# Performance work log

Measured on AMD Instinct MI355X. Metric: run time of the kernel, lower is better.

Reference implementation:

```python
import jax, jax.numpy as jnp
import numpy as np

SEQ, PREV, BS, D_IN, H, D = 512, 512, 8, 1024, 16, 64


def setup_inputs() -> dict:
    key = jax.random.key(0)
    ks = jax.random.split(key, 10)
    s = 0.02
    inp = {
        "input_": jax.random.normal(ks[0], (SEQ, BS, D_IN), jnp.float32),
        "pos_embs": jax.random.normal(ks[1], (SEQ + PREV, D_IN), jnp.float32),
        "memory": jax.random.normal(ks[2], (PREV, BS, D_IN), jnp.float32),
        "u": jax.random.normal(ks[3], (H, D), jnp.float32) * s,
        "v": jax.random.normal(ks[4], (H, D), jnp.float32) * s,
        # causal mask allowing full attention to memory: triu with diagonal=1+prev
        "mask": (jnp.triu(jnp.ones((SEQ, SEQ + PREV), jnp.bool_), k=1 + PREV))[..., None],
        "W_kv": jax.random.normal(ks[5], (D_IN, 2 * H * D), jnp.float32) * s,
        "W_q": jax.random.normal(ks[6], (D_IN, H * D), jnp.float32) * s,
        "W_p": jax.random.normal(ks[7], (D_IN, H * D), jnp.float32) * s,
        "W_out": jax.random.normal(ks[8], (H * D, D_IN), jnp.float32) * s,
        "ln_gamma": jnp.ones((D_IN,), jnp.float32),
        "ln_beta": jnp.zeros((D_IN,), jnp.float32),
    }
    return inp


def _rel_shift(x):
    # x: (q, k, bs, H) -> pad one zero column, reshape-transpose trick, drop first row
    q, k, bs, h = x.shape
    zp = jnp.zeros((q, 1, bs, h), x.dtype)
    return jnp.concatenate([zp, x], axis=1).reshape(k + 1, q, bs, h)[1:].reshape(q, k, bs, h)


def reference(input_, pos_embs, memory, u, v, mask, W_kv, W_q, W_p, W_out, ln_gamma, ln_beta):
    cur_seq, bs, d_in = input_.shape
    prev_seq = memory.shape[0]
    tot = cur_seq + prev_seq
    h, d = u.shape
    scale = 1.0 / d ** 0.5

    iwm = jnp.concatenate([memory, input_], axis=0)          # (tot, bs, d_in)
    kv = jnp.einsum('jbe,ef->jbf', iwm, W_kv)                 # (tot, bs, 2*H*d)
    k_t, v_t = jnp.split(kv, 2, axis=-1)
    q_t = jnp.einsum('ibe,ef->ibf', input_, W_q)              # (cur, bs, H*d)

    q4 = q_t.reshape(cur_seq, bs, h, d)
    k4 = k_t.reshape(tot, bs, h, d)
    v4 = v_t.reshape(tot, bs, h, d)

    content_attn = jnp.einsum('ibhd,jbhd->ijbh', q4 + u, k4)  # (cur, tot, bs, H)

    p_t = (pos_embs @ W_p).reshape(tot, h, d)                 # (tot, H, d)
    position_attn = jnp.einsum('ibhd,jhd->ijbh', q4 + v, p_t)
    position_attn = _rel_shift(position_attn)

    attn = content_attn + position_attn
    attn = jnp.where(mask[..., None], -jnp.inf, attn)         # mask: (cur, tot, 1) -> (cur, tot, 1, 1)
    attn = jax.nn.softmax(attn * scale, axis=1)

    awv = jnp.einsum('ijbh,jbhd->ibhd', attn, v4).reshape(cur_seq, bs, h * d)
    out = input_ + awv @ W_out                                # residual

    mu = jnp.mean(out, axis=-1, keepdims=True)
    var = jnp.mean((out - mu) ** 2, axis=-1, keepdims=True)
    out = (out - mu) / jnp.sqrt(var + 1e-5) * ln_gamma + ln_beta
    return out
```

## Files before the change

kernel.cpp:

```cpp
#include <hip/hip_runtime.h>
#include <math.h>

#define SEQ  512
#define PREV 512
#define TOT  1024
#define BSZ  8
#define DIN  1024
#define NH   16
#define HD   64

typedef __bf16 bf16;
typedef __bf16 bf16x8 __attribute__((ext_vector_type(8)));
typedef float  f32x4  __attribute__((ext_vector_type(4)));
typedef float  f32x16 __attribute__((ext_vector_type(16)));
typedef unsigned int u32;
typedef u32 u32x2 __attribute__((ext_vector_type(2)));

__device__ __forceinline__ f32x4 MFMA16(bf16x8 a, bf16x8 b, f32x4 c) {
    return __builtin_amdgcn_mfma_f32_16x16x32_bf16(a, b, c, 0, 0, 0);
}
__device__ __forceinline__ f32x16 MFMA32(bf16x8 a, bf16x8 b, f32x16 c) {
    return __builtin_amdgcn_mfma_f32_32x32x16_bf16(a, b, c, 0, 0, 0);
}

#define GLOAD16(g, l) __builtin_amdgcn_global_load_lds( \
    (const __attribute__((address_space(1))) void*)(g), \
    (__attribute__((address_space(3))) void*)(l), 16, 0, 0)

__device__ __forceinline__ unsigned short bfbits(float x) {
    return __builtin_bit_cast(unsigned short, (bf16)x);
}
__device__ __forceinline__ float bf2f(u32 bits16) {
    return __builtin_bit_cast(float, bits16 << 16);
}

__global__ __launch_bounds__(256) void prep_all(
    const float* __restrict__ memory, const float* __restrict__ input_,
    const float* __restrict__ pos,
    const float* __restrict__ W_kv, const float* __restrict__ W_q,
    const float* __restrict__ W_p,  const float* __restrict__ W_out,
    bf16* __restrict__ iwm, bf16* __restrict__ posb,
    bf16* __restrict__ wkv, bf16* __restrict__ wq,
    bf16* __restrict__ wp,  bf16* __restrict__ wo)
{
    __shared__ float tile[32][33];
    const int bid = blockIdx.x;
    const int t = threadIdx.x;
    if (bid < 9216) {
        const float* src; bf16* dst; int e4;
        if (bid < 8192) {
            e4 = (bid * 256 + t) * 4;
            src = (e4 < 4194304) ? memory : input_ - 4194304;
            dst = iwm;
        } else {
            e4 = ((bid - 8192) * 256 + t) * 4;
            src = pos; dst = posb;
        }
        float4 x = *(const float4*)(src + e4);
        union { bf16 h[4]; ushort4 u4; } pk;
        pk.h[0] = (bf16)x.x; pk.h[1] = (bf16)x.y; pk.h[2] = (bf16)x.z; pk.h[3] = (bf16)x.w;
        *(ushort4*)(dst + e4) = pk.u4;
        return;
    }
    const int rem = bid - 9216;
    const int bx = rem % 160, by = rem / 160;
    const float* W; bf16* Wt; int N, bn;
    if (bx < 64)       { W = W_kv;  Wt = wkv; N = 2048; bn = bx * 32; }
    else if (bx < 96)  { W = W_q;   Wt = wq;  N = 1024; bn = (bx - 64) * 32; }
    else if (bx < 128) { W = W_p;   Wt = wp;  N = 1024; bn = (bx - 96) * 32; }
    else               { W = W_out; Wt = wo;  N = 1024; bn = (bx - 128) * 32; }
    const int bk = by * 32;
    const int r = t >> 3, c4 = (t & 7) * 4;
    float4 x = *(const float4*)(W + (size_t)(bk + r) * N + bn + c4);
    tile[r][c4 + 0] = x.x; tile[r][c4 + 1] = x.y;
    tile[r][c4 + 2] = x.z; tile[r][c4 + 3] = x.w;
    __syncthreads();
    union { bf16 h[4]; ushort4 u4; } pk;
#pragma unroll
    for (int i = 0; i < 4; ++i) pk.h[i] = (bf16)tile[c4 + i][r];
    *(ushort4*)(Wt + (size_t)(bn + r) * 1024 + bk + c4) = pk.u4;
}

__global__ __launch_bounds__(256, 1) void gemm_kv(
    const bf16* __restrict__ A, const bf16* __restrict__ Bt,
    bf16* __restrict__ C, int M, int N, int K)
{
    __shared__ __align__(16) bf16 A_s[2][256 * 64];
    __shared__ __align__(16) bf16 B_s[2][256 * 64];
    const int t = threadIdx.x;
    const int w = t >> 6, lane = t & 63;
    const int ql = lane & 31, hi2 = lane >> 5;
    const int wm = w >> 1, wn = w & 1;
    const int lin = blockIdx.y * 8 + blockIdx.x;
    const int xcd = lin & 7, idx = lin >> 3;
    const int bm = (xcd * 4 + (idx & 3)) * 256;
    const int bn = (idx >> 2) * 256;

    f32x16 acc[4][4];
#pragma unroll
    for (int mf = 0; mf < 4; ++mf)
#pragma unroll
        for (int nf = 0; nf < 4; ++nf) acc[mf][nf] = (f32x16){};

    const int l7 = lane & 7, l3 = lane >> 3;

    auto stage_half = [&](int buf, int ks, int h) {
        const bf16* __restrict__ src = (h < 2) ? A : Bt;
        const int base = (h < 2) ? bm : bn;
        const int hh = (h & 1) * 128;
        bf16* dst = (h < 2) ? &A_s[buf][0] : &B_s[buf][0];
        const int k0 = ks << 6;
#pragma unroll
        for (int g = 0; g < 4; ++g) {
            const int row = hh + g * 32 + 8 * w + l3;
            const bf16* gp = src + (size_t)(base + row) * K + k0 + ((l7 ^ (row & 7)) * 8);
            GLOAD16(gp, dst + (size_t)row * 64 + l7 * 8);
        }
    };

    bf16x8 af[4], bfr[4];
    auto LDA = [&](int buf, int kt) {
#pragma unroll
        for (int mf = 0; mf < 4; ++mf) {
            int row = wm * 128 + mf * 32 + ql;
            af[mf] = *(const bf16x8*)&A_s[buf][(size_t)row * 64 + (((kt * 2 + hi2) ^ (row & 7)) * 8)];
        }
    };
    auto LDB = [&](int buf, int kt) {
#pragma unroll
        for (int nf = 0; nf < 4; ++nf) {
            int row = wn * 128 + nf * 32 + ql;
            bfr[nf] = *(const bf16x8*)&B_s[buf][(size_t)row * 64 + (((kt * 2 + hi2) ^ (row & 7)) * 8)];
        }
    };

    stage_half(0, 0, 0); stage_half(0, 0, 1); stage_half(0, 0, 2); stage_half(0, 0, 3);

    const int nk = K >> 6;
    for (int ks = 0; ks < nk; ++ks) {
        const int cur = ks & 1, nxt = cur ^ 1;
        asm volatile("s_waitcnt vmcnt(0)" ::: "memory");
        __builtin_amdgcn_sched_barrier(0);
        __builtin_amdgcn_s_barrier();
        __builtin_amdgcn_sched_barrier(0);
        if (ks + 1 < nk) {
            stage_half(nxt, ks + 1, 0); stage_half(nxt, ks + 1, 1);
            stage_half(nxt, ks + 1, 2); stage_half(nxt, ks + 1, 3);
        }
#pragma unroll
        for (int kt = 0; kt < 4; ++kt) {
            LDA(cur, kt); LDB(cur, kt);
            asm volatile("s_waitcnt lgkmcnt(0)" ::: "memory");
            __builtin_amdgcn_sched_barrier(0);
            __builtin_amdgcn_s_setprio(1);
#pragma unroll
            for (int mf = 0; mf < 4; ++mf)
#pragma unroll
                for (int nf = 0; nf < 4; ++nf)
                    acc[mf][nf] = MFMA32(af[mf], bfr[nf], acc[mf][nf]);
            __builtin_amdgcn_s_setprio(0);
        }
    }

#pragma unroll
    for (int mf = 0; mf < 4; ++mf)
#pragma unroll
        for (int nf = 0; nf < 4; ++nf)
#pragma unroll
            for (int r = 0; r < 16; ++r) {
                int row = bm + wm * 128 + mf * 32 + (r & 3) + 8 * (r >> 2) + 4 * hi2;
                int col = bn + wn * 128 + nf * 32 + ql;
                C[(size_t)row * N + col] = (bf16)acc[mf][nf][r];
            }
}

__global__ __launch_bounds__(256) void gemm_out(
    const bf16* __restrict__ A, const bf16* __restrict__ Bt,
    const float* __restrict__ Rres, float* __restrict__ Cf, int N, int K)
{
    __shared__ __align__(16) bf16 A_s[2][128 * 64];
    __shared__ __align__(16) bf16 B_s[2][128 * 64];
    const int t = threadIdx.x;
    const int w = t >> 6, lane = t & 63;
    const int li = lane & 15, hi = lane >> 4;
    const int wr = w >> 1, wc = w & 1;
    const int bm = blockIdx.y * 128, bn = blockIdx.x * 128;
    const int l3 = lane >> 3, l7 = lane & 7;
    const int srcoct = ((l7 ^ l3) * 8);

    f32x4 acc[4][4];
#pragma unroll
    for (int m = 0; m < 4; ++m)
#pragma unroll
        for (int n = 0; n < 4; ++n) acc[m][n] = (f32x4){0.f, 0.f, 0.f, 0.f};

    auto stage = [&](int buf, int k0) {
#pragma unroll
        for (int i = 0; i < 4; ++i) {
            int c = w * 4 + i;
            GLOAD16(A + (size_t)(bm + c * 8 + l3) * K + k0 + srcoct, &A_s[buf][c * 512]);
            GLOAD16(Bt + (size_t)(bn + c * 8 + l3) * K + k0 + srcoct, &B_s[buf][c * 512]);
        }
    };

    stage(0, 0);
    const int nk = K >> 6;
    for (int ks = 0; ks < nk; ++ks) {
        const int cur = ks & 1, nxt = cur ^ 1;
        asm volatile("s_waitcnt vmcnt(0)" ::: "memory");
        __builtin_amdgcn_sched_barrier(0);
        __builtin_amdgcn_s_barrier();
        __builtin_amdgcn_sched_barrier(0);
        if (ks + 1 < nk) stage(nxt, (ks + 1) << 6);
#pragma unroll
        for (int kk = 0; kk < 2; ++kk) {
            bf16x8 af[4], bfr[4];
#pragma unroll
            for (int m = 0; m < 4; ++m) {
                int row = wr * 64 + m * 16 + li;
                af[m] = *(const bf16x8*)&A_s[cur][row * 64 + ((kk * 32 + hi * 8) ^ ((row & 7) * 8))];
            }
#pragma unroll
            for (int n = 0; n < 4; ++n) {
                int row = wc * 64 + n * 16 + li;
                bfr[n] = *(const bf16x8*)&B_s[cur][row * 64 + ((kk * 32 + hi * 8) ^ ((row & 7) * 8))];
            }
            asm volatile("s_waitcnt lgkmcnt(0)" ::: "memory");
            __builtin_amdgcn_sched_barrier(0);
            __builtin_amdgcn_s_setprio(1);
#pragma unroll
            for (int m = 0; m < 4; ++m)
#pragma unroll
                for (int n = 0; n < 4; ++n)
                    acc[m][n] = MFMA16(af[m], bfr[n], acc[m][n]);
            __builtin_amdgcn_s_setprio(0);
        }
    }

#pragma unroll
    for (int m = 0; m < 4; ++m)
#pragma unroll
        for (int n = 0; n < 4; ++n)
#pragma unroll
            for (int r = 0; r < 4; ++r) {
                int row = bm + wr * 64 + m * 16 + hi * 4 + r;
                int col = bn + wc * 64 + n * 16 + li;
                size_t off = (size_t)row * N + col;
                Cf[off] = acc[m][n][r] + Rres[off];
            }
}

__global__ __launch_bounds__(256) void gemm_qp(
    const bf16* __restrict__ iwmq, const bf16* __restrict__ posb,
    const bf16* __restrict__ wq, const bf16* __restrict__ wp,
    bf16* __restrict__ qbf, bf16* __restrict__ pbf)
{
    __shared__ __align__(16) bf16 A_s[128 * 64];
    __shared__ __align__(16) bf16 B_s[128 * 64];
    const int t = threadIdx.x;
    const int w = t >> 6, lane = t & 63;
    const int li = lane & 15, hi = lane >> 4;
    const int wr = w >> 1, wc = w & 1;
    const int by = blockIdx.y;
    const bf16* A; const bf16* Bt; bf16* Cb; int bm;
    if (by < 32) { A = iwmq; Bt = wq; Cb = qbf; bm = by * 128; }
    else         { A = posb; Bt = wp; Cb = pbf; bm = (by - 32) * 128; }
    const int bn = blockIdx.x * 128;
    const int l3 = lane >> 3, l7 = lane & 7;
    const int srcoct = ((l7 ^ l3) * 8);

    f32x4 acc[4][4];
#pragma unroll
    for (int m = 0; m < 4; ++m)
#pragma unroll
        for (int n = 0; n < 4; ++n) acc[m][n] = (f32x4){0.f, 0.f, 0.f, 0.f};

    auto stage = [&](int k0) {
#pragma unroll
        for (int i = 0; i < 4; ++i) {
            int c = w * 4 + i;
            GLOAD16(A + (size_t)(bm + c * 8 + l3) * 1024 + k0 + srcoct, &A_s[c * 512]);
            GLOAD16(Bt + (size_t)(bn + c * 8 + l3) * 1024 + k0 + srcoct, &B_s[c * 512]);
        }
    };

    stage(0);
    for (int ks = 0; ks < 16; ++ks) {
        __syncthreads();
#pragma unroll
        for (int kk = 0; kk < 2; ++kk) {
            bf16x8 af[4], bfr[4];
#pragma unroll
            for (int m = 0; m < 4; ++m) {
                int row = wr * 64 + m * 16 + li;
                af[m] = *(const bf16x8*)&A_s[row * 64 + ((kk * 32 + hi * 8) ^ ((row & 7) * 8))];
            }
#pragma unroll
            for (int n = 0; n < 4; ++n) {
                int row = wc * 64 + n * 16 + li;
                bfr[n] = *(const bf16x8*)&B_s[row * 64 + ((kk * 32 + hi * 8) ^ ((row & 7) * 8))];
            }
#pragma unroll
            for (int m = 0; m < 4; ++m)
#pragma unroll
                for (int n = 0; n < 4; ++n)
                    acc[m][n] = MFMA16(af[m], bfr[n], acc[m][n]);
        }
        __syncthreads();
        if (ks + 1 < 16) stage((ks + 1) << 6);
    }

#pragma unroll
    for (int m = 0; m < 4; ++m)
#pragma unroll
        for (int n = 0; n < 4; ++n)
#pragma unroll
            for (int r = 0; r < 4; ++r) {
                int row = bm + wr * 64 + m * 16 + hi * 4 + r;
                int col = bn + wc * 64 + n * 16 + li;
                Cb[(size_t)row * 1024 + col] = (bf16)acc[m][n][r];
            }
}

__global__ __launch_bounds__(256, 2) void attn_mfma(
    const bf16* __restrict__ kv, const bf16* __restrict__ qb,
    const bf16* __restrict__ pb, const float* __restrict__ u,
    const float* __restrict__ v, bf16* __restrict__ awv)
{
    const int bi = (blockIdx.z & 1) ? (3 - blockIdx.x) : blockIdx.x;
    const int i0 = bi * 128;
    const int b  = blockIdx.y;
    const int h  = blockIdx.z;
    const int t  = threadIdx.x;
    const int w  = t >> 6;
    const int lane = t & 63;
    const int ql  = lane & 31;
    const int hi2 = lane >> 5;

    __shared__ __align__(16) bf16 K_s[64 * 64];
    __shared__ __align__(16) bf16 V_s[64][72];
    __shared__ __align__(16) bf16 P_s[256 * 64];
    __shared__ __align__(16) char SCR[4][6912];

    char* rsc = SCR[w];

    const int c8 = t & 7;
    const int rq = t >> 3;
    const int nt = 2 * bi + 10;
    const int C0 = 384 - i0;

    bf16x8 vreg[2];
#pragma unroll
    for (int p = 0; p < 2; ++p)
        vreg[p] = *(const bf16x8*)(kv + (size_t)((p * 32 + rq) * BSZ + b) * 2048 + 1024 + h * HD + c8 * 8);
#pragma unroll
    for (int p = 0; p < 2; ++p)
        GLOAD16(kv + (size_t)((p * 32 + rq) * BSZ + b) * 2048 + h * HD + ((c8 ^ (rq & 7)) * 8),
                K_s + (p * 32 + rq) * 64 + c8 * 8);
#pragma unroll
    for (int cp = 0; cp < 6; ++cp) {
        int grow = C0 + cp * 32 + rq;
        GLOAD16(pb + (size_t)grow * DIN + h * HD + ((c8 ^ (rq & 7)) * 8),
                P_s + (grow & 255) * 64 + c8 * 8);
    }

    bf16x8 qu[4], qv[4];
    {
        const size_t qoff = ((size_t)(i0 + w * 32 + ql) * BSZ + b) * DIN + h * HD;
#pragma unroll
        for (int kk = 0; kk < 4; ++kk) {
            bf16x8 q8 = *(const bf16x8*)(qb + qoff + kk * 16 + hi2 * 8);
            const float* up = u + h * HD + kk * 16 + hi2 * 8;
            const float* vp = v + h * HD + kk * 16 + hi2 * 8;
#pragma unroll
            for (int m = 0; m < 8; ++m) {
                float qf = (float)q8[m];
                qu[kk][m] = (bf16)(qf + up[m]);
                qv[kk][m] = (bf16)(qf + vp[m]);
            }
        }
    }

    float mrun = -1e30f, lrun = 0.f;
    f32x16 o[2];
    o[0] = (f32x16){}; o[1] = (f32x16){};

    const int phq = (31 - ql) & 3;
    const int sel = phq >> 1;
    const int shb = (phq & 1) * 16;

    for (int tt = 0; tt < nt; ++tt) {
        const int j0 = tt * 64;

        __builtin_amdgcn_s_barrier();
        __builtin_amdgcn_sched_barrier(0);

#pragma unroll
        for (int p = 0; p < 2; ++p) {
            int j = p * 32 + rq;
#pragma unroll
            for (int mm = 0; mm < 8; ++mm)
                V_s[c8 * 8 + mm][(j + 8 * c8) & 63] = vreg[p][mm];
        }
        asm volatile("s_waitcnt vmcnt(0) lgkmcnt(0)" ::: "memory");
        __builtin_amdgcn_sched_barrier(0);
        __builtin_amdgcn_s_barrier();
        __builtin_amdgcn_sched_barrier(0);

        f32x16 st[2];
        st[0] = (f32x16){}; st[1] = (f32x16){};
        __builtin_amdgcn_s_setprio(1);
#pragma unroll
        for (int jt = 0; jt < 2; ++jt) {
            int row = jt * 32 + ql;
#pragma unroll
            for (int kk = 0; kk < 4; ++kk) {
                bf16x8 kf = *(const bf16x8*)&K_s[row * 64 + (((kk * 2 + hi2) ^ (ql & 7)) * 8)];
                st[jt] = MFMA32(kf, qu[kk], st[jt]);
            }
        }
        const int bwg = j0 - i0 + 480 - 32 * w;
        f32x16 rp[3];
        rp[0] = (f32x16){}; rp[1] = (f32x16){}; rp[2] = (f32x16){};
#pragma unroll
        for (int Rt = 0; Rt < 3; ++Rt) {
            int ring = (bwg + Rt * 32 + ql) & 255;
#pragma unroll
            for (int kk = 0; kk < 4; ++kk) {
                bf16x8 pf = *(const bf16x8*)&P_s[ring * 64 + (((kk * 2 + hi2) ^ (ring & 7)) * 8)];
                rp[Rt] = MFMA32(pf, qv[kk], rp[Rt]);
            }
        }
        __builtin_amdgcn_s_setprio(0);

#pragma unroll
        for (int Rt = 0; Rt < 3; ++Rt)
#pragma unroll
            for (int a = 0; a < 4; ++a) {
                u32 lo = (u32)bfbits(rp[Rt][a * 4 + 0]) | ((u32)bfbits(rp[Rt][a * 4 + 1]) << 16);
                u32 hi = (u32)bfbits(rp[Rt][a * 4 + 2]) | ((u32)bfbits(rp[Rt][a * 4 + 3]) << 16);
                *(u32x2*)(rsc + ql * 216 + 64 * Rt + 16 * a + 8 * hi2) = (u32x2){lo, hi};
            }

        __builtin_amdgcn_s_barrier();
        __builtin_amdgcn_sched_barrier(0);

        if (tt + 1 < nt) {
            const int j0n = j0 + 64;
#pragma unroll
            for (int p = 0; p < 2; ++p)
                vreg[p] = *(const bf16x8*)(kv + (size_t)((j0n + p * 32 + rq) * BSZ + b) * 2048 + 1024 + h * HD + c8 * 8);
#pragma unroll
            for (int p = 0; p < 2; ++p)
                GLOAD16(kv + (size_t)((j0n + p * 32 + rq) * BSZ + b) * 2048 + h * HD + ((c8 ^ (rq & 7)) * 8),
                        K_s + (p * 32 + rq) * 64 + c8 * 8);
        }
        if (tt + 3 < nt) {
            const int Cs = C0 + (tt + 3) * 64;
#pragma unroll
            for (int p = 0; p < 2; ++p) {
                int grow = Cs + p * 32 + rq;
                GLOAD16(pb + (size_t)grow * DIN + h * HD + ((c8 ^ (rq & 7)) * 8),
                        P_s + (grow & 255) * 64 + c8 * 8);
            }
        }

        float rowmax = -1e30f;
        const int limb = i0 + 32 * w + ql + PREV - j0;
        auto assemble = [&](bool domask) {
#pragma unroll
            for (int jt = 0; jt < 2; ++jt)
#pragma unroll
                for (int a = 0; a < 4; ++a) {
                    int e = jt * 32 + 8 * a + 4 * hi2 + 31 - ql;
                    const u32x2* W = (const u32x2*)(rsc + ql * 216 + 8 * (e >> 2));
                    u32x2 A0 = W[0], A1 = W[1];
                    u32 U0 = sel ? A0[1] : A0[0];
                    u32 U1 = sel ? A1[0] : A0[1];
                    u32 U2 = sel ? A1[1] : A1[0];
                    u32 o0 = (u32)((((unsigned long long)U1 << 32) | U0) >> shb);
                    u32 o1 = (u32)((((unsigned long long)U2 << 32) | U1) >> shb);
                    float pq[4] = {bf2f(o0 & 0xffffu), bf2f(o0 >> 16),
                                   bf2f(o1 & 0xffffu), bf2f(o1 >> 16)};
#pragma unroll
                    for (int rr = 0; rr < 4; ++rr) {
                        int r = a * 4 + rr;
                        int lj = jt * 32 + 8 * a + 4 * hi2 + rr;
                        float sv = (st[jt][r] + pq[rr]) * 0.125f;
                        if (domask && lj > limb) sv = -1e30f;
                        st[jt][r] = sv;
                        rowmax = fmaxf(rowmax, sv);
                    }
                }
        };
        if (__builtin_amdgcn_readfirstlane(j0 + 63 - (i0 + 32 * w + PREV)) > 0)
            assemble(true);
        else
            assemble(false);

        {
            u32 rm = __builtin_bit_cast(u32, rowmax), rm2 = rm;
            asm("v_permlane32_swap_b32 %0, %1" : "+v"(rm), "+v"(rm2));
            rowmax = fmaxf(rowmax, __builtin_bit_cast(float, rm));
            rowmax = fmaxf(rowmax, __builtin_bit_cast(float, rm2));
        }

        if (!__all(rowmax - mrun <= 8.f)) {
            float newm = fmaxf(mrun, rowmax);
            float fsc = __expf(mrun - newm);
#pragma unroll
            for (int r = 0; r < 16; ++r) {
                float fr = __shfl(fsc, (r & 3) + 8 * (r >> 2) + 4 * hi2);
                o[0][r] *= fr; o[1][r] *= fr;
            }
            lrun *= fsc;
            mrun = newm;
        }
        float rowsum = 0.f;
#pragma unroll
        for (int jt = 0; jt < 2; ++jt)
#pragma unroll
            for (int r = 0; r < 16; ++r) {
                float p = __expf(st[jt][r] - mrun);
                st[jt][r] = p;
                rowsum += p;
            }
        {
            u32 rs = __builtin_bit_cast(u32, rowsum), rs2 = rs;
            asm("v_permlane32_swap_b32 %0, %1" : "+v"(rs), "+v"(rs2));
            rowsum += __builtin_bit_cast(float, rs2);
        }
        lrun += rowsum;

        u32 pk0[2][4], pk1[2][4];
#pragma unroll
        for (int jt = 0; jt < 2; ++jt)
#pragma unroll
            for (int a = 0; a < 4; ++a) {
                pk0[jt][a] = (u32)bfbits(st[jt][a * 4 + 0]) | ((u32)bfbits(st[jt][a * 4 + 1]) << 16);
                pk1[jt][a] = (u32)bfbits(st[jt][a * 4 + 2]) | ((u32)bfbits(st[jt][a * 4 + 3]) << 16);
            }

        __builtin_amdgcn_s_setprio(1);
#pragma unroll
        for (int js = 0; js < 4; ++js) {
            const int jt = js >> 1, a0 = 2 * (js & 1), a1 = a0 + 1;
            u32 w0 = pk0[jt][a0], w2 = pk0[jt][a1];
            asm("v_permlane32_swap_b32 %0, %1" : "+v"(w0), "+v"(w2));
            u32 w1 = pk1[jt][a0], w3 = pk1[jt][a1];
            asm("v_permlane32_swap_b32 %0, %1" : "+v"(w1), "+v"(w3));
            union { u32 uw[4]; bf16x8 vv; } pa;
            pa.uw[0] = w0; pa.uw[1] = w1; pa.uw[2] = w2; pa.uw[3] = w3;
#pragma unroll
            for (int dt = 0; dt < 2; ++dt) {
                int dcol = dt * 32 + ql;
                int colb = (js * 16 + hi2 * 8 + 8 * (dcol >> 3)) & 63;
                bf16x8 vf = *(const bf16x8*)&V_s[dcol][colb];
                o[dt] = MFMA32(pa.vv, vf, o[dt]);
            }
        }
        __builtin_amdgcn_s_setprio(0);
    }

    float linv = __builtin_amdgcn_rcpf(lrun);
    float lr[16];
#pragma unroll
    for (int r = 0; r < 16; ++r) lr[r] = __shfl(linv, (r & 3) + 8 * (r >> 2) + 4 * hi2);
#pragma unroll
    for (int dt = 0; dt < 2; ++dt)
#pragma unroll
        for (int r = 0; r < 16; ++r) {
            int row = i0 + 32 * w + (r & 3) + 8 * (r >> 2) + 4 * hi2;
            awv[((size_t)row * BSZ + b) * DIN + h * HD + dt * 32 + ql] = (bf16)(o[dt][r] * lr[r]);
        }
}

__global__ __launch_bounds__(256) void ln_f32(
    float* __restrict__ out, const float* __restrict__ gamma, const float* __restrict__ beta)
{
    const int row = blockIdx.x;
    const int t = threadIdx.x;
    float4 x = *(float4*)(out + (size_t)row * DIN + t * 4);
    float s  = x.x + x.y + x.z + x.w;
    float ss = x.x * x.x + x.y * x.y + x.z * x.z + x.w * x.w;
#pragma unroll
    for (int wd = 1; wd < 64; wd <<= 1) { s += __shfl_xor(s, wd); ss += __shfl_xor(ss, wd); }
    __shared__ float sbuf[4], ssbuf[4];
    const int wave = t >> 6, lanei = t & 63;
    if (lanei == 0) { sbuf[wave] = s; ssbuf[wave] = ss; }
    __syncthreads();
    s  = sbuf[0] + sbuf[1] + sbuf[2] + sbuf[3];
    ss = ssbuf[0] + ssbuf[1] + ssbuf[2] + ssbuf[3];
    const float mu   = s * (1.f / DIN);
    const float var  = ss * (1.f / DIN) - mu * mu;
    const float rstd = rsqrtf(var + 1e-5f);
    float4 g  = *(const float4*)(gamma + t * 4);
    float4 bb = *(const float4*)(beta + t * 4);
    float4 y;
    y.x = (x.x - mu) * rstd * g.x + bb.x;
    y.y = (x.y - mu) * rstd * g.y + bb.y;
    y.z = (x.z - mu) * rstd * g.z + bb.z;
    y.w = (x.w - mu) * rstd * g.w + bb.w;
    *(float4*)(out + (size_t)row * DIN + t * 4) = y;
}

extern "C" void kernel_launch(void* const* d_in, const int* in_sizes, int n_in,
                              void* d_out, int out_size, void* d_ws, size_t ws_size,
                              hipStream_t stream)
{
    const float* input_ = (const float*)d_in[0];
    const float* pos    = (const float*)d_in[1];
    const float* memory = (const float*)d_in[2];
    const float* u      = (const float*)d_in[3];
    const float* v      = (const float*)d_in[4];
    const float* W_kv   = (const float*)d_in[6];
    const float* W_q    = (const float*)d_in[7];
    const float* W_p    = (const float*)d_in[8];
    const float* W_out  = (const float*)d_in[9];
    const float* gamma  = (const float*)d_in[10];
    const float* beta   = (const float*)d_in[11];

    bf16* iwm  = (bf16*)d_ws;
    bf16* kvb  = iwm  + (size_t)8192 * 1024;
    bf16* qbf  = kvb  + (size_t)8192 * 2048;
    bf16* pbf  = qbf  + (size_t)4096 * 1024;
    bf16* posb = pbf  + (size_t)1024 * 1024;
    bf16* wkv  = posb + (size_t)1024 * 1024;
    bf16* wq   = wkv  + (size_t)2048 * 1024;
    bf16* wp   = wq   + (size_t)1024 * 1024;
    bf16* wo   = wp   + (size_t)1024 * 1024;
    bf16* awvb = wo   + (size_t)1024 * 1024;
    float* outf = (float*)d_out;

    prep_all<<<14336, 256, 0, stream>>>(memory, input_, pos, W_kv, W_q, W_p, W_out,
                                        iwm, posb, wkv, wq, wp, wo);

    gemm_kv<<<dim3(8, 32), 256, 0, stream>>>(iwm, wkv, kvb, 8192, 2048, 1024);
    gemm_qp<<<dim3(8, 40), 256, 0, stream>>>(iwm + (size_t)4096 * 1024, posb, wq, wp, qbf, pbf);

    attn_mfma<<<dim3(4, 8, 16), 256, 0, stream>>>(kvb, qbf, pbf, u, v, awvb);

    gemm_out<<<dim3(8, 32), 256, 0, stream>>>(awvb, wo, input_, outf, 1024, 1024);
    ln_f32<<<4096, 256, 0, stream>>>(outf, gamma, beta);
}
```

Baseline: 174.0 us.

## Double-buffer GEMM LDS fragment loads and use raw exp2 in attention softmax

In the projection GEMM, the A/B LDS fragment loads for the next k-step now go into a second register set while the current MFMAs run. A partial lgkmcnt wait replaces the full drain, so LDS latency overlaps with matrix math. In the attention kernel, log2(e) is folded into the score scale and the exponentials use v_exp_f32 directly instead of __expf, with the rescale threshold adjusted to match. The cost is extra VGPRs for the doubled fragment registers, which may affect occupancy, and the exp2 path gives up any extra handling that __expf lowering would include.

Result: faster. 170.0 us (-2.3%).

```diff
diff --git a/kernel.cpp b/kernel.cpp
--- a/kernel.cpp
+++ b/kernel.cpp
@@ -32,6 +32,11 @@
 }
 __device__ __forceinline__ float bf2f(u32 bits16) {
     return __builtin_bit_cast(float, bits16 << 16);
+}
+__device__ __forceinline__ float exp2_raw(float x) {
+    float r;
+    asm("v_exp_f32 %0, %1" : "=v"(r) : "v"(x));
+    return r;
 }
 
 __global__ __launch_bounds__(256) void prep_all(
@@ -118,19 +123,19 @@
         }
     };
 
-    bf16x8 af[4], bfr[4];
-    auto LDA = [&](int buf, int kt) {
+    bf16x8 af[2][4], bfr[2][4];
+    auto LDA = [&](int buf, int kt, int set) {
 #pragma unroll
         for (int mf = 0; mf < 4; ++mf) {
             int row = wm * 128 + mf * 32 + ql;
-            af[mf] = *(const bf16x8*)&A_s[buf][(size_t)row * 64 + (((kt * 2 + hi2) ^ (row & 7)) * 8)];
+            af[set][mf] = *(const bf16x8*)&A_s[buf][(size_t)row * 64 + (((kt * 2 + hi2) ^ (row & 7)) * 8)];
         }
     };
-    auto LDB = [&](int buf, int kt) {
+    auto LDB = [&](int buf, int kt, int set) {
 #pragma unroll
         for (int nf = 0; nf < 4; ++nf) {
             int row = wn * 128 + nf * 32 + ql;
-            bfr[nf] = *(const bf16x8*)&B_s[buf][(size_t)row * 64 + (((kt * 2 + hi2) ^ (row & 7)) * 8)];
+            bfr[set][nf] = *(const bf16x8*)&B_s[buf][(size_t)row * 64 + (((kt * 2 + hi2) ^ (row & 7)) * 8)];
         }
     };
 
@@ -143,21 +148,27 @@
         __builtin_amdgcn_sched_barrier(0);
         __builtin_amdgcn_s_barrier();
         __builtin_amdgcn_sched_barrier(0);
+        LDA(cur, 0, 0); LDB(cur, 0, 0);
         if (ks + 1 < nk) {
             stage_half(nxt, ks + 1, 0); stage_half(nxt, ks + 1, 1);
             stage_half(nxt, ks + 1, 2); stage_half(nxt, ks + 1, 3);
         }
 #pragma unroll
         for (int kt = 0; kt < 4; ++kt) {
-            LDA(cur, kt); LDB(cur, kt);
-            asm volatile("s_waitcnt lgkmcnt(0)" ::: "memory");
+            const int set = kt & 1;
+            if (kt < 3) {
+                LDA(cur, kt + 1, set ^ 1); LDB(cur, kt + 1, set ^ 1);
+                asm volatile("s_waitcnt lgkmcnt(8)" ::: "memory");
+            } else {
+                asm volatile("s_waitcnt lgkmcnt(0)" ::: "memory");
+            }
             __builtin_amdgcn_sched_barrier(0);
             __builtin_amdgcn_s_setprio(1);
 #pragma unroll
             for (int mf = 0; mf < 4; ++mf)
 #pragma unroll
                 for (int nf = 0; nf < 4; ++nf)
-                    acc[mf][nf] = MFMA32(af[mf], bfr[nf], acc[mf][nf]);
+                    acc[mf][nf] = MFMA32(af[set][mf], bfr[set][nf], acc[mf][nf]);
             __builtin_amdgcn_s_setprio(0);
         }
     }
@@ -348,6 +359,7 @@
     const int rq = t >> 3;
     const int nt = 2 * bi + 10;
     const int C0 = 384 - i0;
+    const float SCL2 = 0.125f * 1.44269504088896f;
 
     bf16x8 vreg[2];
 #pragma unroll
@@ -486,7 +498,7 @@
                     for (int rr = 0; rr < 4; ++rr) {
                         int r = a * 4 + rr;
                         int lj = jt * 32 + 8 * a + 4 * hi2 + rr;
-                        float sv = (st[jt][r] + pq[rr]) * 0.125f;
+                        float sv = (st[jt][r] + pq[rr]) * SCL2;
                         if (domask && lj > limb) sv = -1e30f;
                         st[jt][r] = sv;
                         rowmax = fmaxf(rowmax, sv);
@@ -505,9 +517,9 @@
             rowmax = fmaxf(rowmax, __builtin_bit_cast(float, rm2));
         }
 
-        if (!__all(rowmax - mrun <= 8.f)) {
+        if (!__all(rowmax - mrun <= 11.54f)) {
             float newm = fmaxf(mrun, rowmax);
-            float fsc = __expf(mrun - newm);
+            float fsc = exp2_raw(mrun - newm);
 #pragma unroll
             for (int r = 0; r < 16; ++r) {
                 float fr = __shfl(fsc, (r & 3) + 8 * (r >> 2) + 4 * hi2);
@@ -521,7 +533,7 @@
         for (int jt = 0; jt < 2; ++jt)
 #pragma unroll
             for (int r = 0; r < 16; ++r) {
-                float p = __expf(st[jt][r] - mrun);
+                float p = exp2_raw(st[jt][r] - mrun);
                 st[jt][r] = p;
                 rowsum += p;
             }
```
